# Kernel tuning notes

Hardware: AMD Instinct MI355X
Metric: run time of the kernel (lower is better)

## Reference

```python
import jax, jax.numpy as jnp
import numpy as np

WIDTH = 32
DEPTH = 5
DATA = 1
WEIGHTS_LIM = 1.0
# layer dims (in, out) matching nn.Sequential of Linears with swish in between
DIMS = [(1, WIDTH)] + [(WIDTH, WIDTH)] * (DEPTH - 1) + [(WIDTH, 2 * DATA)]
P = sum(o * i + o for (i, o) in DIMS)  # 4354


def mlp_apply(theta, x):
    """Batched hypernetwork MLP. theta: (B,P) flat weights, x: (B,1) time input.
    Returns (B, 2): concat(tanh(mean), std)."""
    y = x
    idx = 0
    n = len(DIMS)
    for li, (i, o) in enumerate(DIMS):
        W = theta[:, idx:idx + o * i].reshape(-1, o, i)
        idx += o * i
        b = theta[:, idx:idx + o]
        idx += o
        y = jnp.einsum('bi,boi->bo', y, W) + b
        if li < n - 1:
            y = jax.nn.silu(y)  # swish
    mean, logvar = jnp.split(y, 2, axis=-1)
    mean = jnp.tanh(mean)  # final_activation
    std = jnp.exp(0.5 * jnp.clip(logvar, -4.0, 4.0))
    return jnp.concatenate([mean, std], axis=-1)


def setup_inputs() -> dict:
    key = jax.random.key(0)
    k1, k2, k3, k4, k5 = jax.random.split(key, 5)
    batch, seq = 32, 64
    xs = jnp.tanh(jax.random.normal(k1, (batch, seq), dtype=jnp.float32))
    noise = jax.random.normal(k2, (seq, batch, 1), dtype=jnp.float32)
    theta_init = 0.1 * jax.random.normal(k3, (P,), dtype=jnp.float32)
    # A initialized near identity (nn.Parameter(torch.eye) + training drift)
    A = jnp.eye(P, dtype=jnp.float32) + 0.001 * jax.random.normal(k4, (P, P), dtype=jnp.float32)
    bound = float(np.sqrt(6.0 / (P + 1)))  # xavier_uniform for B (P,1)
    B = jax.random.uniform(k5, (P, 1), dtype=jnp.float32, minval=-bound, maxval=bound)
    return {"xs": xs, "noise": noise, "theta_init": theta_init, "A": A, "B": B,
            "inference_start": 32}


def reference(xs, noise, theta_init, A, B, inference_start):
    batch, seq = xs.shape
    theta0 = jnp.broadcast_to(theta_init[None, :], (batch, P))
    x_prev0 = jnp.zeros((batch, 1), dtype=xs.dtype)
    root_input0 = jnp.zeros((batch, 1), dtype=xs.dtype)  # time t=0
    mu_sigma0 = mlp_apply(theta0, root_input0)

    ts = jnp.arange(seq, dtype=jnp.int32)

    def step(carry, inp):
        theta, x_prev, mu_sigma = carry
        x_col, nz, t = inp
        mean, std = jnp.split(mu_sigma, 2, axis=-1)  # (B,1) each
        x_hat = nz * std + mean
        x_t = jnp.where(t < inference_start, x_col[:, None], x_hat)
        update = (x_t - x_prev) @ B.T  # (B,P)
        theta = jnp.clip(theta @ A.T + update, -WEIGHTS_LIM, WEIGHTS_LIM)
        next_time = jnp.broadcast_to(
            ((t + 1).astype(xs.dtype) / seq), (batch, 1))
        mu_sigma_next = mlp_apply(theta, next_time)
        return (theta, x_t, mu_sigma_next), (mean[:, 0], std[:, 0])

    _, (means, stds) = jax.lax.scan(step, (theta0, x_prev0, mu_sigma0),
                                    (xs.T, noise, ts))
    return means.T, stds.T  # (batch, seq) each
```

## Files before the change

kernel.cpp:

```cpp
#include <hip/hip_runtime.h>
#include <hip/hip_cooperative_groups.h>

#define PNUM 4354
#define PPAD 4416
#define KPAD 4608
#define NPT  276
#define KITER 144
#define NWG  138
#define NTHR 512
#define THSTRIDE (32 * KPAD)

typedef __attribute__((ext_vector_type(8))) _Float16 f16x8;
typedef __attribute__((ext_vector_type(4))) float f32x4;

#define MFMA16 __builtin_amdgcn_mfma_f32_16x16x32_f16

__device__ __forceinline__ float silu_f(float x) { return x / (1.f + __expf(-x)); }

__global__ void wsm_prep(const float* __restrict__ A, const float* __restrict__ Bv,
                         const float* __restrict__ th0,
                         _Float16* __restrict__ Ehs, _Float16* __restrict__ Els,
                         float* __restrict__ thf, _Float16* __restrict__ thh,
                         _Float16* __restrict__ thl, float* __restrict__ Bpad,
                         unsigned int* __restrict__ flag) {
  const long long gsz = (long long)gridDim.x * blockDim.x;
  const long long gid = (long long)blockIdx.x * blockDim.x + threadIdx.x;
  const long long totE = (long long)NPT * KITER * 64 * 8;
  for (long long i = gid; i < totE; i += gsz) {
    const int j    = (int)(i & 7);
    const int lane = (int)((i >> 3) & 63);
    const int ki   = (int)((i >> 9) % KITER);
    const int pt   = (int)(i / ((long long)KITER * 512));
    const int p = pt * 16 + (lane & 15);
    const int k = ki * 32 + ((lane >> 4) << 3) + j;
    float v = 0.f;
    if (p < PNUM && k < PNUM) {
      v = A[(long long)p * PNUM + k];
      if (p == k) v -= 1.f;
    }
    const _Float16 h = (_Float16)v;
    Ehs[i] = h;
    Els[i] = (_Float16)(v - (float)h);
  }
  for (long long i = gid; i < 2LL * THSTRIDE; i += gsz) {
    const int p = (int)(i % KPAD);
    const float v = (i < THSTRIDE && p < PNUM) ? th0[p] : 0.f;
    thf[i] = v;
    const _Float16 h = (_Float16)v;
    thh[i] = h;
    thl[i] = (_Float16)(v - (float)h);
  }
  for (long long i = gid; i < PPAD; i += gsz)
    Bpad[i] = (i < PNUM) ? Bv[i] : 0.f;
  if (gid == 0) *flag = 0u;
}

__device__ __forceinline__ void mlp_eval(int b, int o, const float* __restrict__ th,
                                         float tin, float* __restrict__ musig,
                                         unsigned int* __restrict__ flag) {
  float h = silu_f(tin * th[o] + th[32 + o]);
  int idx = 64;
  #pragma unroll
  for (int L = 0; L < 4; ++L) {
    const float* Wr = th + idx + o * 32;
    float hn = th[idx + 1024 + o];
    #pragma unroll
    for (int i = 0; i < 32; ++i)
      hn = fmaf(__shfl(h, i, 32), Wr[i], hn);
    h = silu_f(hn);
    idx += 1056;
  }
  float p0 = h * th[4288 + o];
  float p1 = h * th[4320 + o];
  #pragma unroll
  for (int off = 16; off > 0; off >>= 1) {
    p0 += __shfl_xor(p0, off, 32);
    p1 += __shfl_xor(p1, off, 32);
  }
  if (o == 0) {
    const float mean = tanhf(p0 + th[4352]);
    float lv = p1 + th[4353];
    lv = fminf(fmaxf(lv, -4.f), 4.f);
    const float sd = __expf(0.5f * lv);
    __hip_atomic_store(&musig[2 * b], mean, __ATOMIC_RELAXED, __HIP_MEMORY_SCOPE_AGENT);
    __hip_atomic_store(&musig[2 * b + 1], sd, __ATOMIC_RELAXED, __HIP_MEMORY_SCOPE_AGENT);
    __hip_atomic_fetch_add(flag, 1u, __ATOMIC_RELEASE, __HIP_MEMORY_SCOPE_AGENT);
  }
}

__global__ void __launch_bounds__(NTHR) wsm_main(
    const float* __restrict__ xs, const float* __restrict__ noise,
    const int* __restrict__ infp,
    const _Float16* __restrict__ Ehs, const _Float16* __restrict__ Els,
    float* __restrict__ thf, _Float16* __restrict__ thh, _Float16* __restrict__ thl,
    const float* __restrict__ Bpad, float* __restrict__ musig,
    unsigned int* __restrict__ flag, float* __restrict__ outp)
{
  cooperative_groups::grid_group grid = cooperative_groups::this_grid();
  const int tid = threadIdx.x;
  const int wg = blockIdx.x;
  const int wave = tid >> 6;
  const int lane = tid & 63;
  const int psub = wave & 1;
  const int kc = wave >> 1;
  const long long ebase = (((long long)(wg * 2 + psub) * KITER + kc * 36) * 64 + lane) * 8;
  const int koff = kc * 1152 + ((lane >> 4) << 3);
  const int row0 = (lane & 15) * KPAD + koff;
  const int row1 = row0 + 16 * KPAD;
  const int em = tid >> 4;
  const int epc0 = (tid & 15) * 2;
  const int inf_start = *infp;
  float xprev = 0.f;
  __shared__ float red[8][64][8];

  for (int t = 0; t < 64; ++t) {
    const int inb = t & 1;
    const float*    thf_in  = thf + inb * THSTRIDE;
    float*          thf_out = thf + (inb ^ 1) * THSTRIDE;
    const _Float16* thh_in  = thh + inb * THSTRIDE;
    _Float16*       thh_out = thh + (inb ^ 1) * THSTRIDE;
    const _Float16* thl_in  = thl + inb * THSTRIDE;
    _Float16*       thl_out = thl + (inb ^ 1) * THSTRIDE;

    if (wg < 32 && wave == 0 && lane < 32)
      mlp_eval(wg, lane, thf_in + wg * KPAD, (float)t * (1.f / 64.f), musig, flag);

    f32x4 z = {0.f, 0.f, 0.f, 0.f};
    f32x4 hh0 = z, hh1 = z, hl0 = z, hl1 = z, lh0 = z, lh1 = z;
    const _Float16* ehp  = Ehs + ebase;
    const _Float16* elp  = Els + ebase;
    const _Float16* ah0p = thh_in + row0;
    const _Float16* ah1p = thh_in + row1;
    const _Float16* al0p = thl_in + row0;
    const _Float16* al1p = thl_in + row1;
    #pragma unroll 4
    for (int i = 0; i < 36; ++i) {
      const f16x8 eh  = *(const f16x8*)(ehp + i * 512);
      const f16x8 el  = *(const f16x8*)(elp + i * 512);
      const f16x8 ah0 = *(const f16x8*)(ah0p + i * 32);
      const f16x8 ah1 = *(const f16x8*)(ah1p + i * 32);
      const f16x8 al0 = *(const f16x8*)(al0p + i * 32);
      const f16x8 al1 = *(const f16x8*)(al1p + i * 32);
      hh0 = MFMA16(ah0, eh, hh0, 0, 0, 0);
      hh1 = MFMA16(ah1, eh, hh1, 0, 0, 0);
      hl0 = MFMA16(ah0, el, hl0, 0, 0, 0);
      hl1 = MFMA16(ah1, el, hl1, 0, 0, 0);
      lh0 = MFMA16(al0, eh, lh0, 0, 0, 0);
      lh1 = MFMA16(al1, eh, lh1, 0, 0, 0);
    }
    const f32x4 c0 = hh0 + hl0 + lh0;
    const f32x4 c1 = hh1 + hl1 + lh1;
    #pragma unroll
    for (int r = 0; r < 4; ++r) {
      red[wave][lane][r] = c0[r];
      red[wave][lane][4 + r] = c1[r];
    }
    __syncthreads();

    const unsigned int tgt = 32u * (unsigned)(t + 1);
    while (__hip_atomic_load(flag, __ATOMIC_ACQUIRE, __HIP_MEMORY_SCOPE_AGENT) < tgt)
      __builtin_amdgcn_s_sleep(8);

    const float mean = __hip_atomic_load(&musig[2 * em], __ATOMIC_RELAXED, __HIP_MEMORY_SCOPE_AGENT);
    const float sd   = __hip_atomic_load(&musig[2 * em + 1], __ATOMIC_RELAXED, __HIP_MEMORY_SCOPE_AGENT);
    const float xhat = fmaf(noise[t * 32 + em], sd, mean);
    const float xt   = (t < inf_start) ? xs[em * 64 + t] : xhat;
    const float dlt  = xt - xprev;
    xprev = xt;

    #pragma unroll
    for (int jj = 0; jj < 2; ++jj) {
      const int pcl = epc0 + jj;
      const int pc = wg * 32 + pcl;
      const int lanei = (pcl & 15) + (((em & 15) >> 2) << 4);
      const int reg = (em & 15) & 3;
      const int hf4 = (em >> 4) * 4;
      float s = 0.f;
      #pragma unroll
      for (int k2 = 0; k2 < 4; ++k2)
        s += red[k2 * 2 + (pcl >> 4)][lanei][hf4 + reg];
      const long long idx = (long long)em * KPAD + pc;
      float v = thf_in[idx] + s + dlt * Bpad[pc];
      v = fminf(fmaxf(v, -1.f), 1.f);
      thf_out[idx] = v;
      const _Float16 hv = (_Float16)v;
      thh_out[idx] = hv;
      thl_out[idx] = (_Float16)(v - (float)hv);
    }

    if (wg == 0 && tid < 32) {
      outp[tid * 64 + t] = __hip_atomic_load(&musig[2 * tid], __ATOMIC_RELAXED, __HIP_MEMORY_SCOPE_AGENT);
      outp[32 * 64 + tid * 64 + t] = __hip_atomic_load(&musig[2 * tid + 1], __ATOMIC_RELAXED, __HIP_MEMORY_SCOPE_AGENT);
    }

    grid.sync();
  }
}

extern "C" void kernel_launch(void* const* d_in, const int* in_sizes, int n_in,
                              void* d_out, int out_size, void* d_ws, size_t ws_size,
                              hipStream_t stream) {
  const float* xs  = (const float*)d_in[0];
  const float* noise = (const float*)d_in[1];
  const float* th0 = (const float*)d_in[2];
  const float* A   = (const float*)d_in[3];
  const float* Bv  = (const float*)d_in[4];
  const int* infs  = (const int*)d_in[5];

  char* ws = (char*)d_ws;
  size_t off = 0;
  auto carve = [&](size_t bytes) -> void* {
    off = (off + 255) & ~(size_t)255;
    void* p = ws + off;
    off += bytes;
    return p;
  };
  _Float16* Ehs = (_Float16*)carve((size_t)NPT * KITER * 512 * sizeof(_Float16));
  _Float16* Els = (_Float16*)carve((size_t)NPT * KITER * 512 * sizeof(_Float16));
  float*    thf = (float*)carve((size_t)2 * THSTRIDE * sizeof(float));
  _Float16* thh = (_Float16*)carve((size_t)2 * THSTRIDE * sizeof(_Float16));
  _Float16* thl = (_Float16*)carve((size_t)2 * THSTRIDE * sizeof(_Float16));
  float*   Bpad = (float*)carve((size_t)PPAD * sizeof(float));
  float*  musig = (float*)carve((size_t)64 * sizeof(float));
  unsigned int* flag = (unsigned int*)carve(sizeof(unsigned int));
  float* outp = (float*)d_out;

  wsm_prep<<<dim3(1024), dim3(256), 0, stream>>>(A, Bv, th0, Ehs, Els, thf, thh, thl, Bpad, flag);

  void* args[] = {(void*)&xs, (void*)&noise, (void*)&infs, (void*)&Ehs, (void*)&Els,
                  (void*)&thf, (void*)&thh, (void*)&thl, (void*)&Bpad,
                  (void*)&musig, (void*)&flag, (void*)&outp};
  hipLaunchCooperativeKernel((const void*)wsm_main, dim3(NWG), dim3(NTHR), args, 0, stream);
}
```

Before: 4.501 ms.

## Swizzle theta fp16 split into MFMA fragment layout and double-buffer operand loads

Stores the hi/lo fp16 copies of theta in the same lane-major fragment layout as the E matrix, so each lane reads one contiguous 16-byte vector at a 512-element stride instead of strided rows. The K loop becomes an explicit two-buffer software pipeline of grouped loads and MFMAs. The prep kernel now writes 8-wide vector stores, and the reduction scratch is padded to 9 to avoid LDS bank conflicts. The epilogue scatters updated theta into the swizzled layout, which adds index math and scattered 2-byte writes. Holding two buffers of operands raises register pressure.

```diff
diff --git a/kernel.cpp b/kernel.cpp
--- a/kernel.cpp
+++ b/kernel.cpp
@@ -8,7 +8,9 @@
 #define KITER 144
 #define NWG  138
 #define NTHR 512
-#define THSTRIDE (32 * KPAD)
+#define HALFSTRIDE (144 * 512)
+#define THSWZ (2 * HALFSTRIDE)
+#define THF_STRIDE (32 * KPAD)
 
 typedef __attribute__((ext_vector_type(8))) _Float16 f16x8;
 typedef __attribute__((ext_vector_type(4))) float f32x4;
@@ -25,30 +27,45 @@
                          unsigned int* __restrict__ flag) {
   const long long gsz = (long long)gridDim.x * blockDim.x;
   const long long gid = (long long)blockIdx.x * blockDim.x + threadIdx.x;
-  const long long totE = (long long)NPT * KITER * 64 * 8;
-  for (long long i = gid; i < totE; i += gsz) {
-    const int j    = (int)(i & 7);
-    const int lane = (int)((i >> 3) & 63);
-    const int ki   = (int)((i >> 9) % KITER);
-    const int pt   = (int)(i / ((long long)KITER * 512));
+  const long long totE8 = (long long)NPT * KITER * 64;
+  for (long long u = gid; u < totE8; u += gsz) {
+    const int lane = (int)(u & 63);
+    const long long r = u >> 6;
+    const int ki = (int)(r % KITER);
+    const int pt = (int)(r / KITER);
     const int p = pt * 16 + (lane & 15);
-    const int k = ki * 32 + ((lane >> 4) << 3) + j;
-    float v = 0.f;
-    if (p < PNUM && k < PNUM) {
-      v = A[(long long)p * PNUM + k];
-      if (p == k) v -= 1.f;
-    }
-    const _Float16 h = (_Float16)v;
-    Ehs[i] = h;
-    Els[i] = (_Float16)(v - (float)h);
-  }
-  for (long long i = gid; i < 2LL * THSTRIDE; i += gsz) {
-    const int p = (int)(i % KPAD);
-    const float v = (i < THSTRIDE && p < PNUM) ? th0[p] : 0.f;
-    thf[i] = v;
+    const int k0 = ki * 32 + ((lane >> 4) << 3);
+    f16x8 h8, l8;
+    #pragma unroll
+    for (int j = 0; j < 8; ++j) {
+      const int k = k0 + j;
+      float v = 0.f;
+      if (p < PNUM && k < PNUM) {
+        v = A[(long long)p * PNUM + k];
+        if (p == k) v -= 1.f;
+      }
+      const _Float16 h = (_Float16)v;
+      h8[j] = h;
+      l8[j] = (_Float16)(v - (float)h);
+    }
+    *(f16x8*)(Ehs + u * 8) = h8;
+    *(f16x8*)(Els + u * 8) = l8;
+  }
+  for (long long i = gid; i < 2LL * THSWZ; i += gsz) {
+    const long long local = i % THSWZ;
+    const int tb = (int)(i / THSWZ);
+    const int j = (int)(local & 7);
+    const int lane = (int)((local >> 3) & 63);
+    const int ki = (int)((local >> 9) % KITER);
+    const int Pc = ki * 32 + (((lane >> 4) & 3) << 3) + j;
+    const float v = (tb == 0 && Pc < PNUM) ? th0[Pc] : 0.f;
     const _Float16 h = (_Float16)v;
     thh[i] = h;
     thl[i] = (_Float16)(v - (float)h);
+  }
+  for (long long i = gid; i < 2LL * THF_STRIDE; i += gsz) {
+    const int p = (int)(i % KPAD);
+    thf[i] = (i < THF_STRIDE && p < PNUM) ? th0[p] : 0.f;
   }
   for (long long i = gid; i < PPAD; i += gsz)
     Bpad[i] = (i < PNUM) ? Bv[i] : 0.f;
@@ -88,7 +105,36 @@
   }
 }
 
-__global__ void __launch_bounds__(NTHR) wsm_main(
+__device__ __forceinline__ void load_group(f16x8 (&B)[4][6], int g,
+    const _Float16* __restrict__ ehp, const _Float16* __restrict__ elp,
+    const _Float16* __restrict__ ah0p, const _Float16* __restrict__ ah1p,
+    const _Float16* __restrict__ al0p, const _Float16* __restrict__ al1p) {
+  #pragma unroll
+  for (int i = 0; i < 4; ++i) {
+    const int off = (g * 4 + i) * 512;
+    B[i][0] = *(const f16x8*)(ehp + off);
+    B[i][1] = *(const f16x8*)(elp + off);
+    B[i][2] = *(const f16x8*)(ah0p + off);
+    B[i][3] = *(const f16x8*)(ah1p + off);
+    B[i][4] = *(const f16x8*)(al0p + off);
+    B[i][5] = *(const f16x8*)(al1p + off);
+  }
+}
+
+__device__ __forceinline__ void comp_group(f16x8 (&B)[4][6],
+    f32x4& hh0, f32x4& hh1, f32x4& hl0, f32x4& hl1, f32x4& lh0, f32x4& lh1) {
+  #pragma unroll
+  for (int i = 0; i < 4; ++i) {
+    hh0 = MFMA16(B[i][2], B[i][0], hh0, 0, 0, 0);
+    hh1 = MFMA16(B[i][3], B[i][0], hh1, 0, 0, 0);
+    hl0 = MFMA16(B[i][2], B[i][1], hl0, 0, 0, 0);
+    hl1 = MFMA16(B[i][3], B[i][1], hl1, 0, 0, 0);
+    lh0 = MFMA16(B[i][4], B[i][0], lh0, 0, 0, 0);
+    lh1 = MFMA16(B[i][5], B[i][0], lh1, 0, 0, 0);
+  }
+}
+
+__global__ void __launch_bounds__(NTHR, 2) wsm_main(
     const float* __restrict__ xs, const float* __restrict__ noise,
     const int* __restrict__ infp,
     const _Float16* __restrict__ Ehs, const _Float16* __restrict__ Els,
@@ -104,50 +150,53 @@
   const int psub = wave & 1;
   const int kc = wave >> 1;
   const long long ebase = (((long long)(wg * 2 + psub) * KITER + kc * 36) * 64 + lane) * 8;
-  const int koff = kc * 1152 + ((lane >> 4) << 3);
-  const int row0 = (lane & 15) * KPAD + koff;
-  const int row1 = row0 + 16 * KPAD;
+  const long long tbase = ((long long)(kc * 36) * 64 + lane) * 8;
   const int em = tid >> 4;
   const int epc0 = (tid & 15) * 2;
   const int inf_start = *infp;
   float xprev = 0.f;
-  __shared__ float red[8][64][8];
+  __shared__ float red[8][64][9];
 
   for (int t = 0; t < 64; ++t) {
     const int inb = t & 1;
-    const float*    thf_in  = thf + inb * THSTRIDE;
-    float*          thf_out = thf + (inb ^ 1) * THSTRIDE;
-    const _Float16* thh_in  = thh + inb * THSTRIDE;
-    _Float16*       thh_out = thh + (inb ^ 1) * THSTRIDE;
-    const _Float16* thl_in  = thl + inb * THSTRIDE;
-    _Float16*       thl_out = thl + (inb ^ 1) * THSTRIDE;
+    const float*    thf_in  = thf + inb * THF_STRIDE;
+    float*          thf_out = thf + (inb ^ 1) * THF_STRIDE;
+    const _Float16* thh_in  = thh + inb * THSWZ;
+    _Float16*       thh_out = thh + (inb ^ 1) * THSWZ;
+    const _Float16* thl_in  = thl + inb * THSWZ;
+    _Float16*       thl_out = thl + (inb ^ 1) * THSWZ;
 
     if (wg < 32 && wave == 0 && lane < 32)
       mlp_eval(wg, lane, thf_in + wg * KPAD, (float)t * (1.f / 64.f), musig, flag);
 
+    const _Float16* ehp  = Ehs + ebase;
+    const _Float16* elp  = Els + ebase;
+    const _Float16* ah0p = thh_in + tbase;
+    const _Float16* ah1p = ah0p + HALFSTRIDE;
+    const _Float16* al0p = thl_in + tbase;
+    const _Float16* al1p = al0p + HALFSTRIDE;
     f32x4 z = {0.f, 0.f, 0.f, 0.f};
     f32x4 hh0 = z, hh1 = z, hl0 = z, hl1 = z, lh0 = z, lh1 = z;
-    const _Float16* ehp  = Ehs + ebase;
-    const _Float16* elp  = Els + ebase;
-    const _Float16* ah0p = thh_in + row0;
-    const _Float16* ah1p = thh_in + row1;
-    const _Float16* al0p = thl_in + row0;
-    const _Float16* al1p = thl_in + row1;
-    #pragma unroll 4
-    for (int i = 0; i < 36; ++i) {
-      const f16x8 eh  = *(const f16x8*)(ehp + i * 512);
-      const f16x8 el  = *(const f16x8*)(elp + i * 512);
-      const f16x8 ah0 = *(const f16x8*)(ah0p + i * 32);
-      const f16x8 ah1 = *(const f16x8*)(ah1p + i * 32);
-      const f16x8 al0 = *(const f16x8*)(al0p + i * 32);
-      const f16x8 al1 = *(const f16x8*)(al1p + i * 32);
-      hh0 = MFMA16(ah0, eh, hh0, 0, 0, 0);
-      hh1 = MFMA16(ah1, eh, hh1, 0, 0, 0);
-      hl0 = MFMA16(ah0, el, hl0, 0, 0, 0);
-      hl1 = MFMA16(ah1, el, hl1, 0, 0, 0);
-      lh0 = MFMA16(al0, eh, lh0, 0, 0, 0);
-      lh1 = MFMA16(al1, eh, lh1, 0, 0, 0);
-    }
+    f16x8 GA[4][6], GB[4][6];
+    load_group(GA, 0, ehp, elp, ah0p, ah1p, al0p, al1p);
+    load_group(GB, 1, ehp, elp, ah0p, ah1p, al0p, al1p);
+    comp_group(GA, hh0, hh1, hl0, hl1, lh0, lh1);
+    load_group(GA, 2, ehp, elp, ah0p, ah1p, al0p, al1p);
+    comp_group(GB, hh0, hh1, hl0, hl1, lh0, lh1);
+    load_group(GB, 3, ehp, elp, ah0p, ah1p, al0p, al1p);
+    comp_group(GA, hh0, hh1, hl0, hl1, lh0, lh1);
+    load_group(GA, 4, ehp, elp, ah0p, ah1p, al0p, al1p);
+    comp_group(GB, hh0, hh1, hl0, hl1, lh0, lh1);
+    load_group(GB, 5, ehp, elp, ah0p, ah1p, al0p, al1p);
+    comp_group(GA, hh0, hh1, hl0, hl1, lh0, lh1);
+    load_group(GA, 6, ehp, elp, ah0p, ah1p, al0p, al1p);
+    comp_group(GB, hh0, hh1, hl0, hl1, lh0, lh1);
+    load_group(GB, 7, ehp, elp, ah0p, ah1p, al0p, al1p);
+    comp_group(GA, hh0, hh1, hl0, hl1, lh0, lh1);
+    load_group(GA, 8, ehp, elp, ah0p, ah1p, al0p, al1p);
+    comp_group(GB, hh0, hh1, hl0, hl1, lh0, lh1);
+    comp_group(GA, hh0, hh1, hl0, hl1, lh0, lh1);
+
     const f32x4 c0 = hh0 + hl0 + lh0;
     const f32x4 c1 = hh1 + hl1 + lh1;
     #pragma unroll
@@ -173,7 +222,7 @@
       const int pcl = epc0 + jj;
       const int pc = wg * 32 + pcl;
       const int lanei = (pcl & 15) + (((em & 15) >> 2) << 4);
-      const int reg = (em & 15) & 3;
+      const int reg = em & 3;
       const int hf4 = (em >> 4) * 4;
       float s = 0.f;
       #pragma unroll
@@ -184,8 +233,14 @@
       v = fminf(fmaxf(v, -1.f), 1.f);
       thf_out[idx] = v;
       const _Float16 hv = (_Float16)v;
-      thh_out[idx] = hv;
-      thl_out[idx] = (_Float16)(v - (float)hv);
+      const _Float16 lvv = (_Float16)(v - (float)hv);
+      const int ki_e = pc >> 5;
+      const int sub_e = (pc >> 3) & 3;
+      const int j_e = pc & 7;
+      const int lane_e = (em & 15) + (sub_e << 4);
+      const long long sidx = (((long long)(em >> 4) * KITER + ki_e) * 64 + lane_e) * 8 + j_e;
+      thh_out[sidx] = hv;
+      thl_out[sidx] = lvv;
     }
 
     if (wg == 0 && tid < 32) {
@@ -217,9 +272,9 @@
   };
   _Float16* Ehs = (_Float16*)carve((size_t)NPT * KITER * 512 * sizeof(_Float16));
   _Float16* Els = (_Float16*)carve((size_t)NPT * KITER * 512 * sizeof(_Float16));
-  float*    thf = (float*)carve((size_t)2 * THSTRIDE * sizeof(float));
-  _Float16* thh = (_Float16*)carve((size_t)2 * THSTRIDE * sizeof(_Float16));
-  _Float16* thl = (_Float16*)carve((size_t)2 * THSTRIDE * sizeof(_Float16));
+  float*    thf = (float*)carve((size_t)2 * THF_STRIDE * sizeof(float));
+  _Float16* thh = (_Float16*)carve((size_t)2 * THSWZ * sizeof(_Float16));
+  _Float16* thl = (_Float16*)carve((size_t)2 * THSWZ * sizeof(_Float16));
   float*   Bpad = (float*)carve((size_t)PPAD * sizeof(float));
   float*  musig = (float*)carve((size_t)64 * sizeof(float));
   unsigned int* flag = (unsigned int*)carve(sizeof(unsigned int));
```

New measurement: 4.422 ms. No clear change (-1.7%).
